# Optimization experiments

Measured on AMD Instinct MI355X. Metric: run time of the kernel, lower is better.

## Reference

```python
import jax, jax.numpy as jnp
import numpy as np


def setup_inputs() -> dict:
    key = jax.random.key(0)
    ks = jax.random.split(key, 7)
    SEQ, B, IN, H, OUT = 1024, 1024, 57, 128, 18
    return {
        "line_tensor": jax.random.normal(ks[0], (SEQ, B, IN), dtype=jnp.float32),
        "W_ih": jax.random.normal(ks[1], (H, IN), dtype=jnp.float32) * 0.1,
        "b_ih": jax.random.normal(ks[2], (H,), dtype=jnp.float32) * 0.1,
        "W_hh": jax.random.normal(ks[3], (H, H), dtype=jnp.float32) * 0.1,
        "b_hh": jax.random.normal(ks[4], (H,), dtype=jnp.float32) * 0.1,
        "W_ho": jax.random.normal(ks[5], (OUT, H), dtype=jnp.float32) * 0.1,
        "b_ho": jax.random.normal(ks[6], (OUT,), dtype=jnp.float32) * 0.1,
    }


def reference(line_tensor, W_ih, b_ih, W_hh, b_hh, W_ho, b_ho):
    # Elman RNN: h_t = tanh(i2h(x_t) + h2h(h_{t-1})); output = log_softmax(h2o(h_T))
    B = line_tensor.shape[1]
    H = W_hh.shape[0]
    h0 = jnp.zeros((B, H), dtype=line_tensor.dtype)

    def step(h, x):  # x: [B, IN], h: [B, H]
        h = jnp.tanh(x @ W_ih.T + b_ih + h @ W_hh.T + b_hh)
        return h, None

    hT, _ = jax.lax.scan(step, h0, line_tensor)
    logits = hT @ W_ho.T + b_ho  # [B, OUT]
    out = jax.nn.log_softmax(logits, axis=1)
    return (out, hT)
```

## Files before the change

### kernel.cpp

```cpp
#include <hip/hip_runtime.h>
#include <math.h>

#define SEQ   1024
#define BATCH 1024
#define IN_F  57
#define H_F   128
#define OUT_F 18
#define MROWS 16
#define HSTR  136
#define XSTR  72

typedef __attribute__((ext_vector_type(8))) short bf8;
typedef __attribute__((ext_vector_type(4))) float f32x4;

static __device__ __forceinline__ short f2bf(float f) {
    unsigned u = __builtin_bit_cast(unsigned, f);
    u = (u + 0x7FFFu + ((u >> 16) & 1u)) >> 16;
    return (short)u;
}
static __device__ __forceinline__ float bf2f(short s) {
    unsigned u = ((unsigned)(unsigned short)s) << 16;
    return __builtin_bit_cast(float, u);
}

__global__ __launch_bounds__(256) void rnn_mfma_kernel(
    const float* __restrict__ X,
    const float* __restrict__ W_ih,
    const float* __restrict__ b_ih,
    const float* __restrict__ W_hh,
    const float* __restrict__ b_hh,
    const float* __restrict__ W_ho,
    const float* __restrict__ b_ho,
    float* __restrict__ out)
{
    const int tid  = threadIdx.x;
    const int lane = tid & 63;
    const int wv   = tid >> 6;
    const int n16  = lane & 15;
    const int quad = lane >> 4;
    const int b0   = blockIdx.x * MROWS;

    __shared__ short h_lds[2][MROWS][HSTR];
    __shared__ short x_lds[2][MROWS][XSTR];
    __shared__ float logits_lds[MROWS][OUT_F];
    __shared__ float red_lds[MROWS][2];

    const int j0 = wv * 32 + n16;
    const int j1 = j0 + 16;

    const float* wp0 = W_hh + j0 * H_F + quad * 8;
    const float* wp1 = W_hh + j1 * H_F + quad * 8;
#define LDW8(P) ({ \
        f32x4 p_ = *(const f32x4*)(P); \
        f32x4 q_ = *(const f32x4*)((P) + 4); \
        bf8 f_; \
        f_[0]=f2bf(p_[0]); f_[1]=f2bf(p_[1]); f_[2]=f2bf(p_[2]); f_[3]=f2bf(p_[3]); \
        f_[4]=f2bf(q_[0]); f_[5]=f2bf(q_[1]); f_[6]=f2bf(q_[2]); f_[7]=f2bf(q_[3]); \
        f_; })
    bf8 wh00 = LDW8(wp0 +  0), wh01 = LDW8(wp0 + 32), wh02 = LDW8(wp0 + 64), wh03 = LDW8(wp0 + 96);
    bf8 wh10 = LDW8(wp1 +  0), wh11 = LDW8(wp1 + 32), wh12 = LDW8(wp1 + 64), wh13 = LDW8(wp1 + 96);

#define LDWI(J, KS) ({ \
        bf8 f_; \
        _Pragma("unroll") \
        for (int i_ = 0; i_ < 8; ++i_) { \
            int k_ = (KS) * 32 + quad * 8 + i_; \
            f_[i_] = (k_ < IN_F) ? f2bf(W_ih[(J) * IN_F + k_]) : (short)0; \
        } f_; })
    bf8 wi00 = LDWI(j0, 0), wi01 = LDWI(j0, 1), wi10 = LDWI(j1, 0), wi11 = LDWI(j1, 1);

    const float bias0 = b_ih[j0] + b_hh[j0];
    const float bias1 = b_ih[j1] + b_hh[j1];

    for (int i = tid; i < MROWS * HSTR; i += 256) (&h_lds[0][0][0])[i] = 0;
    for (int i = tid; i < 2 * MROWS * XSTR; i += 256) (&x_lds[0][0][0])[i] = 0;
    if (tid < 228) {
        f32x4 v = *(const f32x4*)(X + (size_t)b0 * IN_F + tid * 4);
        #pragma unroll
        for (int e = 0; e < 4; ++e) {
            int idx = tid * 4 + e;
            int m = (int)((unsigned)idx / 57u);
            int k = idx - m * 57;
            x_lds[0][m][k] = f2bf(v[e]);
        }
    }
    __syncthreads();

    const size_t tstride = (size_t)BATCH * IN_F;

#define MFMA __builtin_amdgcn_mfma_f32_16x16x32_bf16
#define STEP(CB, NB, T) do { \
        f32x4 xp = {0.f, 0.f, 0.f, 0.f}; \
        const bool pre = ((T) + 1 < SEQ) && (tid < 228); \
        if (pre) xp = *(const f32x4*)(X + (size_t)((T) + 1) * tstride + (size_t)b0 * IN_F + tid * 4); \
        const short* hc = &h_lds[CB][0][0] + n16 * HSTR + quad * 8; \
        const short* xc = &x_lds[CB][0][0] + n16 * XSTR + quad * 8; \
        bf8 ah0 = *(const bf8*)(hc +  0); \
        bf8 ah1 = *(const bf8*)(hc + 32); \
        bf8 ah2 = *(const bf8*)(hc + 64); \
        bf8 ah3 = *(const bf8*)(hc + 96); \
        bf8 ax0 = *(const bf8*)(xc +  0); \
        bf8 ax1 = *(const bf8*)(xc + 32); \
        f32x4 c0 = {bias0, bias0, bias0, bias0}; \
        f32x4 c1 = {bias1, bias1, bias1, bias1}; \
        c0 = MFMA(ah0, wh00, c0, 0, 0, 0); \
        c1 = MFMA(ah0, wh10, c1, 0, 0, 0); \
        c0 = MFMA(ah1, wh01, c0, 0, 0, 0); \
        c1 = MFMA(ah1, wh11, c1, 0, 0, 0); \
        c0 = MFMA(ah2, wh02, c0, 0, 0, 0); \
        c1 = MFMA(ah2, wh12, c1, 0, 0, 0); \
        c0 = MFMA(ah3, wh03, c0, 0, 0, 0); \
        c1 = MFMA(ah3, wh13, c1, 0, 0, 0); \
        c0 = MFMA(ax0, wi00, c0, 0, 0, 0); \
        c1 = MFMA(ax0, wi10, c1, 0, 0, 0); \
        c0 = MFMA(ax1, wi01, c0, 0, 0, 0); \
        c1 = MFMA(ax1, wi11, c1, 0, 0, 0); \
        short* hn = &h_lds[NB][0][0]; \
        _Pragma("unroll") \
        for (int r = 0; r < 4; ++r) { \
            int m = quad * 4 + r;   \
            float z0 = fminf(fmaxf(c0[r], -9.f), 9.f); \
            float e0 = __expf(2.f * z0); \
            hn[m * HSTR + j0] = f2bf((e0 - 1.f) * __builtin_amdgcn_rcpf(e0 + 1.f)); \
            float z1 = fminf(fmaxf(c1[r], -9.f), 9.f); \
            float e1 = __expf(2.f * z1); \
            hn[m * HSTR + j1] = f2bf((e1 - 1.f) * __builtin_amdgcn_rcpf(e1 + 1.f)); \
        } \
        if (pre) { \
            _Pragma("unroll") \
            for (int e = 0; e < 4; ++e) { \
                int idx = tid * 4 + e; \
                int m = (int)((unsigned)idx / 57u); \
                int k = idx - m * 57; \
                x_lds[NB][m][k] = f2bf(xp[e]); \
            } \
        } \
        __syncthreads(); \
    } while (0)

    for (int t = 0; t < SEQ; t += 2) { STEP(0, 1, t); STEP(1, 0, t + 1); }
#undef STEP
#undef MFMA

    float* hT = out + (size_t)BATCH * OUT_F;
    #pragma unroll
    for (int r = 0; r < (MROWS * H_F) / 256; ++r) {
        int idx = tid + r * 256;
        int m = idx >> 7, k = idx & 127;
        hT[(size_t)(b0 + m) * H_F + k] = bf2f(h_lds[0][m][k]);
    }

    for (int idx = tid; idx < MROWS * OUT_F; idx += 256) {
        int m = idx / OUT_F, o = idx - m * OUT_F;
        float acc = b_ho[o];
        for (int k = 0; k < H_F; ++k)
            acc = fmaf(bf2f(h_lds[0][m][k]), W_ho[o * H_F + k], acc);
        logits_lds[m][o] = acc;
    }
    __syncthreads();

    if (tid < MROWS) {
        float mx = -1e30f;
        #pragma unroll
        for (int o = 0; o < OUT_F; ++o) mx = fmaxf(mx, logits_lds[tid][o]);
        float s = 0.f;
        #pragma unroll
        for (int o = 0; o < OUT_F; ++o) s += expf(logits_lds[tid][o] - mx);
        red_lds[tid][0] = mx;
        red_lds[tid][1] = logf(s);
    }
    __syncthreads();

    for (int idx = tid; idx < MROWS * OUT_F; idx += 256) {
        int m = idx / OUT_F, o = idx - m * OUT_F;
        out[(size_t)(b0 + m) * OUT_F + o] =
            logits_lds[m][o] - red_lds[m][0] - red_lds[m][1];
    }
}

extern "C" void kernel_launch(void* const* d_in, const int* in_sizes, int n_in,
                              void* d_out, int out_size, void* d_ws, size_t ws_size,
                              hipStream_t stream) {
    const float* X    = (const float*)d_in[0];
    const float* W_ih = (const float*)d_in[1];
    const float* b_ih = (const float*)d_in[2];
    const float* W_hh = (const float*)d_in[3];
    const float* b_hh = (const float*)d_in[4];
    const float* W_ho = (const float*)d_in[5];
    const float* b_ho = (const float*)d_in[6];
    float* out = (float*)d_out;

    rnn_mfma_kernel<<<dim3(BATCH / MROWS), dim3(256), 0, stream>>>(
        X, W_ih, b_ih, W_hh, b_hh, W_ho, b_ho, out);
}
```

Before: 891.1 us.

## Prefetch X two steps ahead and split MFMA accumulator chains

Input rows are now loaded from global memory two timesteps ahead into two rotating register buffers, so each global load has a full step of latency hiding before it is written to LDS. The x_lds store for the next step moves before the MFMAs, and the LDS index math (division by 57) is precomputed once outside the loop. Each output tile now uses two independent accumulator chains that are summed before tanh, which shortens the dependent MFMA chain. The cost is extra registers for the second accumulator pair and the prefetch buffer.

```diff
diff --git a/kernel.cpp b/kernel.cpp
--- a/kernel.cpp
+++ b/kernel.cpp
@@ -72,27 +72,32 @@
     const float bias0 = b_ih[j0] + b_hh[j0];
     const float bias1 = b_ih[j1] + b_hh[j1];
 
+    const bool  xlane = (tid < 228);
+    const size_t tstride = (size_t)BATCH * IN_F;
+    const float* xbase = X + (size_t)b0 * IN_F + tid * 4;
+    int xm[4], xk[4];
+    #pragma unroll
+    for (int e = 0; e < 4; ++e) {
+        int idx = tid * 4 + e;
+        xm[e] = (int)((unsigned)idx / 57u);
+        xk[e] = idx - xm[e] * 57;
+    }
+
     for (int i = tid; i < MROWS * HSTR; i += 256) (&h_lds[0][0][0])[i] = 0;
     for (int i = tid; i < 2 * MROWS * XSTR; i += 256) (&x_lds[0][0][0])[i] = 0;
-    if (tid < 228) {
-        f32x4 v = *(const f32x4*)(X + (size_t)b0 * IN_F + tid * 4);
+    f32x4 xq0 = {0,0,0,0}, xq1 = {0,0,0,0};
+    if (xlane) {
+        f32x4 v = *(const f32x4*)(xbase);
         #pragma unroll
-        for (int e = 0; e < 4; ++e) {
-            int idx = tid * 4 + e;
-            int m = (int)((unsigned)idx / 57u);
-            int k = idx - m * 57;
-            x_lds[0][m][k] = f2bf(v[e]);
-        }
+        for (int e = 0; e < 4; ++e) x_lds[0][xm[e]][xk[e]] = f2bf(v[e]);
+        xq1 = *(const f32x4*)(xbase + 1 * tstride);
+        xq0 = *(const f32x4*)(xbase + 2 * tstride);
     }
     __syncthreads();
 
-    const size_t tstride = (size_t)BATCH * IN_F;
-
 #define MFMA __builtin_amdgcn_mfma_f32_16x16x32_bf16
-#define STEP(CB, NB, T) do { \
-        f32x4 xp = {0.f, 0.f, 0.f, 0.f}; \
-        const bool pre = ((T) + 1 < SEQ) && (tid < 228); \
-        if (pre) xp = *(const f32x4*)(X + (size_t)((T) + 1) * tstride + (size_t)b0 * IN_F + tid * 4); \
+#define STEP(CB, NB, T, XS) do { \
+         \
         const short* hc = &h_lds[CB][0][0] + n16 * HSTR + quad * 8; \
         const short* xc = &x_lds[CB][0][0] + n16 * XSTR + quad * 8; \
         bf8 ah0 = *(const bf8*)(hc +  0); \
@@ -101,44 +106,47 @@
         bf8 ah3 = *(const bf8*)(hc + 96); \
         bf8 ax0 = *(const bf8*)(xc +  0); \
         bf8 ax1 = *(const bf8*)(xc + 32); \
-        f32x4 c0 = {bias0, bias0, bias0, bias0}; \
-        f32x4 c1 = {bias1, bias1, bias1, bias1}; \
-        c0 = MFMA(ah0, wh00, c0, 0, 0, 0); \
-        c1 = MFMA(ah0, wh10, c1, 0, 0, 0); \
-        c0 = MFMA(ah1, wh01, c0, 0, 0, 0); \
-        c1 = MFMA(ah1, wh11, c1, 0, 0, 0); \
-        c0 = MFMA(ah2, wh02, c0, 0, 0, 0); \
-        c1 = MFMA(ah2, wh12, c1, 0, 0, 0); \
-        c0 = MFMA(ah3, wh03, c0, 0, 0, 0); \
-        c1 = MFMA(ah3, wh13, c1, 0, 0, 0); \
-        c0 = MFMA(ax0, wi00, c0, 0, 0, 0); \
-        c1 = MFMA(ax0, wi10, c1, 0, 0, 0); \
-        c0 = MFMA(ax1, wi01, c0, 0, 0, 0); \
-        c1 = MFMA(ax1, wi11, c1, 0, 0, 0); \
+         \
+        if (((T) + 1 < SEQ) && xlane) { \
+            _Pragma("unroll") \
+            for (int e = 0; e < 4; ++e) x_lds[NB][xm[e]][xk[e]] = f2bf(XS[e]); \
+        } \
+         \
+        if (((T) + 3 < SEQ) && xlane) \
+            XS = *(const f32x4*)(xbase + (size_t)((T) + 3) * tstride); \
+         \
+        f32x4 c0a = {bias0, bias0, bias0, bias0}, c0b = {0.f, 0.f, 0.f, 0.f}; \
+        f32x4 c1a = {bias1, bias1, bias1, bias1}, c1b = {0.f, 0.f, 0.f, 0.f}; \
+        c0a = MFMA(ah0, wh00, c0a, 0, 0, 0); \
+        c1a = MFMA(ah0, wh10, c1a, 0, 0, 0); \
+        c0b = MFMA(ah1, wh01, c0b, 0, 0, 0); \
+        c1b = MFMA(ah1, wh11, c1b, 0, 0, 0); \
+        c0a = MFMA(ah2, wh02, c0a, 0, 0, 0); \
+        c1a = MFMA(ah2, wh12, c1a, 0, 0, 0); \
+        c0b = MFMA(ah3, wh03, c0b, 0, 0, 0); \
+        c1b = MFMA(ah3, wh13, c1b, 0, 0, 0); \
+        c0a = MFMA(ax0, wi00, c0a, 0, 0, 0); \
+        c1a = MFMA(ax0, wi10, c1a, 0, 0, 0); \
+        c0b = MFMA(ax1, wi01, c0b, 0, 0, 0); \
+        c1b = MFMA(ax1, wi11, c1b, 0, 0, 0); \
         short* hn = &h_lds[NB][0][0]; \
         _Pragma("unroll") \
         for (int r = 0; r < 4; ++r) { \
-            int m = quad * 4 + r;   \
-            float z0 = fminf(fmaxf(c0[r], -9.f), 9.f); \
+            int m = quad * 4 + r; \
+            float z0 = fminf(fmaxf(c0a[r] + c0b[r], -9.f), 9.f); \
             float e0 = __expf(2.f * z0); \
             hn[m * HSTR + j0] = f2bf((e0 - 1.f) * __builtin_amdgcn_rcpf(e0 + 1.f)); \
-            float z1 = fminf(fmaxf(c1[r], -9.f), 9.f); \
+            float z1 = fminf(fmaxf(c1a[r] + c1b[r], -9.f), 9.f); \
             float e1 = __expf(2.f * z1); \
             hn[m * HSTR + j1] = f2bf((e1 - 1.f) * __builtin_amdgcn_rcpf(e1 + 1.f)); \
         } \
-        if (pre) { \
-            _Pragma("unroll") \
-            for (int e = 0; e < 4; ++e) { \
-                int idx = tid * 4 + e; \
-                int m = (int)((unsigned)idx / 57u); \
-                int k = idx - m * 57; \
-                x_lds[NB][m][k] = f2bf(xp[e]); \
-            } \
-        } \
         __syncthreads(); \
     } while (0)
 
-    for (int t = 0; t < SEQ; t += 2) { STEP(0, 1, t); STEP(1, 0, t + 1); }
+    for (int t = 0; t < SEQ; t += 2) {
+        STEP(0, 1, t,     xq1);
+        STEP(1, 0, t + 1, xq0);
+    }
 #undef STEP
 #undef MFMA
 
```

Result: faster. 841.9 us (-5.5%).
